# Optimization experiments

Measured on AMD Instinct MI355X. Metric: run time of the kernel, lower is better.

The kernel has to match this reference:

```python
import jax, jax.numpy as jnp
import numpy as np

T = 2048        # q_len (current chunk)
P = 2048        # past KV cache length
HID = 4096      # hidden_size
H = 32          # num_attention_heads
D = HID // H    # head_dim = 128
THETA = 10000.0


def apply_rope(x, pos):
    # x: [H, T, D], pos: [T] int
    half = D // 2
    inv_freq = 1.0 / (THETA ** (jnp.arange(0, half, dtype=jnp.float32) / half))
    ang = pos.astype(jnp.float32)[:, None] * inv_freq[None, :]      # [T, D/2]
    cos = jnp.concatenate([jnp.cos(ang), jnp.cos(ang)], axis=-1)[None]  # [1, T, D]
    sin = jnp.concatenate([jnp.sin(ang), jnp.sin(ang)], axis=-1)[None]
    rot = jnp.concatenate([-x[..., half:], x[..., :half]], axis=-1)
    return x * cos + rot * sin


def setup_inputs() -> dict:
    key = jax.random.key(0)
    ks = jax.random.split(key, 8)
    s = 1.0 / np.sqrt(HID)
    inp = {
        "hidden_states": jax.random.normal(ks[0], (T, HID), dtype=jnp.float32),
        "attention_mask": jnp.triu(jnp.full((T, T), -jnp.inf, dtype=jnp.float32), k=1),
        "Wq": jax.random.normal(ks[1], (HID, HID), dtype=jnp.float32) * s,
        "Wk": jax.random.normal(ks[2], (HID, HID), dtype=jnp.float32) * s,
        "Wv": jax.random.normal(ks[3], (HID, HID), dtype=jnp.float32) * s,
        "Wo": jax.random.normal(ks[4], (HID, HID), dtype=jnp.float32) * s,
        "past_k": jax.random.normal(ks[5], (H, P, D), dtype=jnp.float32),
        "past_v": jax.random.normal(ks[6], (H, P, D), dtype=jnp.float32),
        "position_ids": P + jnp.arange(T, dtype=jnp.int32),
        "past_length": P,
    }
    return inp


def reference(hidden_states, attention_mask, Wq, Wk, Wv, Wo, past_k, past_v,
              position_ids, past_length):
    # QKV projections -> [H, T, D]
    proj = lambda W: (hidden_states @ W).reshape(T, H, D).transpose(1, 0, 2)
    q, k, v = proj(Wq), proj(Wk), proj(Wv)
    q = apply_rope(q, position_ids)
    k = apply_rope(k, position_ids)

    scale = 1.0 / jnp.sqrt(jnp.float32(D))
    # scores against past cache and current chunk (fp32 softmax, as in source)
    past_dots = (jnp.einsum('htd,hsd->hts', q, past_k) * scale).astype(jnp.float32)
    pmask = jnp.where(jnp.arange(P) < past_length, 0.0, -jnp.inf)  # [P]
    past_dots = past_dots + pmask
    cur = ((jnp.einsum('htd,hsd->hts', q, k) * scale) + attention_mask).astype(jnp.float32)

    # online-softmax merge via logsumexp combination
    past_lse = jax.scipy.special.logsumexp(past_dots, axis=-1, keepdims=True)
    cur_lse = jax.scipy.special.logsumexp(cur, axis=-1, keepdims=True)
    tot_lse = jnp.logaddexp(past_lse, cur_lse)
    pw = jnp.exp(past_dots - tot_lse).astype(q.dtype)
    cw = jnp.exp(cur - tot_lse).astype(q.dtype)

    out = jnp.einsum('hts,hsd->htd', pw, past_v) + jnp.einsum('hts,hsd->htd', cw, v)
    out = jnp.where(past_length == 0,
                    jnp.einsum('hts,hsd->htd', jax.nn.softmax(cur, axis=-1).astype(q.dtype), v),
                    out)
    out = out.transpose(1, 0, 2).reshape(T, HID)   # [T, hidden]
    return out @ Wo
```

## Files before the change

### kernel.cpp

```cpp
#include <hip/hip_runtime.h>
#include <cstdint>
#include <cstddef>

#define T_LEN 2048
#define PAST_MAX 2048
#define HID 4096
#define NHEAD 32
#define DHEAD 128

typedef __bf16 bf16_t;
typedef __bf16 bf16x4 __attribute__((ext_vector_type(4)));
typedef __bf16 bf16x8 __attribute__((ext_vector_type(8)));
typedef float  f32x4  __attribute__((ext_vector_type(4)));
typedef float  f32x16 __attribute__((ext_vector_type(16)));
typedef unsigned int u32x4 __attribute__((ext_vector_type(4)));

__device__ __forceinline__ void gload16(const void* g, void* l){
  __builtin_amdgcn_global_load_lds((const __attribute__((address_space(1))) void*)g,
                                   (__attribute__((address_space(3))) void*)l,
                                   16, 0, 0);
}

__device__ __forceinline__ unsigned pack_bf16(float a, float b){
  const unsigned ua = __builtin_bit_cast(unsigned short, (bf16_t)a);
  const unsigned ub = __builtin_bit_cast(unsigned short, (bf16_t)b);
  return ua | (ub << 16);
}

__global__ void cvt2_k(const float* __restrict__ a, bf16_t* __restrict__ ao,
                       const float* __restrict__ b, bf16_t* __restrict__ bo, int n4){
  int i = blockIdx.x * 256 + threadIdx.x;
  if (i < n4){
    const float4 v = ((const float4*)a)[i];
    bf16x4 o = { (bf16_t)v.x, (bf16_t)v.y, (bf16_t)v.z, (bf16_t)v.w };
    ((bf16x4*)ao)[i] = o;
  } else {
    i -= n4;
    const float4 v = ((const float4*)b)[i];
    bf16x4 o = { (bf16_t)v.x, (bf16_t)v.y, (bf16_t)v.z, (bf16_t)v.w };
    ((bf16x4*)bo)[i] = o;
  }
}

__global__ __launch_bounds__(256) void transpose2_k(const float* __restrict__ in,
                                                    bf16_t* __restrict__ out, int R, int C){
  __shared__ float tile[64][65];
  const int r0 = blockIdx.x << 6, c0 = blockIdx.y << 6;
  const size_t bo = (size_t)blockIdx.z * (size_t)R * (size_t)C;
  const int tx = threadIdx.x & 15, ty = threadIdx.x >> 4;
#pragma unroll
  for (int k = 0; k < 4; ++k){
    const float4 v = *(const float4*)(in + bo + (size_t)(r0 + ty + 16*k) * C + c0 + tx*4);
    float* tp = &tile[ty + 16*k][tx*4];
    tp[0] = v.x; tp[1] = v.y; tp[2] = v.z; tp[3] = v.w;
  }
  __syncthreads();
  const int rr0 = (threadIdx.x & 7) * 8;
  const int ccb = threadIdx.x >> 3;
#pragma unroll
  for (int k = 0; k < 2; ++k){
    const int cc = ccb + 32*k;
    bf16x8 o;
#pragma unroll
    for (int j = 0; j < 8; ++j) o[j] = (bf16_t)tile[rr0 + j][cc];
    *(bf16x8*)(out + bo + (size_t)(c0 + cc) * R + r0 + rr0) = o;
  }
}

__global__ __launch_bounds__(256) void transpose3_k(
    const float* __restrict__ s0, const float* __restrict__ s1, const float* __restrict__ s2,
    bf16_t* __restrict__ d0, bf16_t* __restrict__ d1, bf16_t* __restrict__ d2){
  __shared__ float tile[64][65];
  const float* in = (blockIdx.z == 0) ? s0 : (blockIdx.z == 1) ? s1 : s2;
  bf16_t* out = (blockIdx.z == 0) ? d0 : (blockIdx.z == 1) ? d1 : d2;
  const int r0 = blockIdx.x << 6, c0 = blockIdx.y << 6;
  const int tx = threadIdx.x & 15, ty = threadIdx.x >> 4;
#pragma unroll
  for (int k = 0; k < 4; ++k){
    const float4 v = *(const float4*)(in + (size_t)(r0 + ty + 16*k) * HID + c0 + tx*4);
    float* tp = &tile[ty + 16*k][tx*4];
    tp[0] = v.x; tp[1] = v.y; tp[2] = v.z; tp[3] = v.w;
  }
  __syncthreads();
  const int rr0 = (threadIdx.x & 7) * 8;
  const int ccb = threadIdx.x >> 3;
#pragma unroll
  for (int k = 0; k < 2; ++k){
    const int cc = ccb + 32*k;
    bf16x8 o;
#pragma unroll
    for (int j = 0; j < 8; ++j) o[j] = (bf16_t)tile[rr0 + j][cc];
    *(bf16x8*)(out + (size_t)(c0 + cc) * HID + r0 + rr0) = o;
  }
}

__global__ void ropek8_k(bf16_t* __restrict__ K, const int* __restrict__ pos){
  const int idx = blockIdx.x * 256 + threadIdx.x;
  const int jc = idx & 7;
  const int t  = (idx >> 3) & (T_LEN - 1);
  const int h  = idx >> 14;
  const size_t base = ((size_t)h * T_LEN + t) * DHEAD;
  const float p = (float)pos[t];
  bf16x8 lo = *(bf16x8*)(K + base + jc * 8);
  bf16x8 hi = *(bf16x8*)(K + base + 64 + jc * 8);
  bf16x8 olo, ohi;
#pragma unroll
  for (int j = 0; j < 8; ++j){
    const int fi = jc * 8 + j;
    const float invf = __expf(-(float)fi * 0.14391156605212898f);
    float sn, cs;
    sincosf(p * invf, &sn, &cs);
    const float b0 = (float)lo[j], b1 = (float)hi[j];
    olo[j] = (bf16_t)(b0 * cs - b1 * sn);
    ohi[j] = (bf16_t)(b1 * cs + b0 * sn);
  }
  *(bf16x8*)(K + base + jc * 8) = olo;
  *(bf16x8*)(K + base + 64 + jc * 8) = ohi;
}

#define QUAD384(PR, BF) \
  __builtin_amdgcn_s_setprio(1); \
  _Pragma("unroll") \
  for (int kk = 0; kk < 2; ++kk){ \
    _Pragma("unroll") \
    for (int mf = 0; mf < 4; ++mf){ \
      _Pragma("unroll") \
      for (int ni = 0; ni < 2; ++ni) \
        acc[mf][(PR)*2 + ni] = __builtin_amdgcn_mfma_f32_16x16x32_bf16( \
            af[mf][kk], BF[ni][kk], acc[mf][(PR)*2 + ni], 0, 0, 0); \
    } \
  } \
  __builtin_amdgcn_s_setprio(0);

__global__ __launch_bounds__(512, 1) void gemmqkv384_k(
    const bf16_t* __restrict__ A,
    const bf16_t* __restrict__ Bc,
    bf16_t* __restrict__ OQ, bf16_t* __restrict__ OK2, bf16_t* __restrict__ OVT)
{
  const int bid = blockIdx.x;
  const int wg  = (bid & 7) * 64 + (bid >> 3);
  const int mt  = wg & 15;
  const int nt  = wg >> 4;
  const int m0  = mt << 7;
  const int n0g = nt * 384;

  const int tid = threadIdx.x;
  const int wv = tid >> 6, lane = tid & 63, lm = lane & 15, g = lane >> 4;
  const int wr = wv >> 2, wc = wv & 3;

  __shared__ __align__(16) char smem[131072];

  const f32x4 fzero = {0.f, 0.f, 0.f, 0.f};
  f32x4 acc[4][6];
#pragma unroll
  for (int i = 0; i < 4; ++i)
#pragma unroll
    for (int j = 0; j < 6; ++j) acc[i][j] = fzero;

  size_t aoff[2], boff[2];
#pragma unroll
  for (int i = 0; i < 2; ++i){
    const int c = i * 512 + tid;
    const int u = c >> 3;
    const int j = ((c & 7) ^ (u & 7)) << 3;
    aoff[i] = (size_t)(m0 + u) * HID + j;
    const int bcol = (u >> 5) * 96 + (u & 31);
    boff[i] = (size_t)(n0g + bcol) * HID + j;
  }
  const int ldst0 = (wv * 64) << 4;
  const int ldst1 = (512 + wv * 64) << 4;

  auto stgA = [&](char* buf, int kt){
    const bf16_t* src = A + (size_t)kt * 64;
    gload16(src + aoff[0], buf + ldst0);
    gload16(src + aoff[1], buf + ldst1);
  };
  auto stgB = [&](char* buf, int kt, int pr){
    const bf16_t* src = Bc + (size_t)kt * 64 + (size_t)pr * (32 * HID);
    char* dst = buf + 16384 + pr * 16384;
    gload16(src + boff[0], dst + ldst0);
    gload16(src + boff[1], dst + ldst1);
  };

  const int koff0 = ((0 + g) ^ (lm & 7)) << 4;
  const int koff1 = ((4 + g) ^ (lm & 7)) << 4;
  const int abase = ((wr << 6) + lm) << 7;
  const int bbase = ((wc << 5) + lm) << 7;

  stgA(smem, 0); stgB(smem, 0, 0); stgB(smem, 0, 1); stgB(smem, 0, 2);
  stgA(smem + 65536, 1); stgB(smem + 65536, 1, 0); stgB(smem + 65536, 1, 1);
  asm volatile("s_waitcnt vmcnt(6)" ::: "memory");
  __builtin_amdgcn_s_barrier();

  bf16x8 af[4][2], bf[2][2];

  for (int kt = 0; kt < 64; ++kt){
    char* buf  = smem + (kt & 1) * 65536;
    char* obuf = smem + ((kt + 1) & 1) * 65536;

#pragma unroll
    for (int mf = 0; mf < 4; ++mf){
      af[mf][0] = *(const bf16x8*)(buf + abase + mf * 2048 + koff0);
      af[mf][1] = *(const bf16x8*)(buf + abase + mf * 2048 + koff1);
    }
#pragma unroll
    for (int ni = 0; ni < 2; ++ni){
      bf[ni][0] = *(const bf16x8*)(buf + 16384 + bbase + ni * 2048 + koff0);
      bf[ni][1] = *(const bf16x8*)(buf + 16384 + bbase + ni * 2048 + koff1);
    }
    if (kt + 1 < 64) stgB(obuf, kt + 1, 2);
    __builtin_amdgcn_sched_barrier(0);
    __builtin_amdgcn_s_barrier();
    asm volatile("s_waitcnt lgkmcnt(0)" ::: "memory");
    __builtin_amdgcn_sched_barrier(0);
    QUAD384(0, bf)
    __builtin_amdgcn_s_barrier();

#pragma unroll
    for (int ni = 0; ni < 2; ++ni){
      bf[ni][0] = *(const bf16x8*)(buf + 32768 + bbase + ni * 2048 + koff0);
      bf[ni][1] = *(const bf16x8*)(buf + 32768 + bbase + ni * 2048 + koff1);
    }
    if (kt + 2 < 64) stgA(buf, kt + 2);
    __builtin_amdgcn_sched_barrier(0);
    __builtin_amdgcn_s_barrier();
    asm volatile("s_waitcnt lgkmcnt(0)" ::: "memory");
    __builtin_amdgcn_sched_barrier(0);
    QUAD384(1, bf)
    __builtin_amdgcn_s_barrier();

#pragma unroll
    for (int ni = 0; ni < 2; ++ni){
      bf[ni][0] = *(const bf16x8*)(buf + 49152 + bbase + ni * 2048 + koff0);
      bf[ni][1] = *(const bf16x8*)(buf + 49152 + bbase + ni * 2048 + koff1);
    }
    if (kt + 2 < 64){ stgB(buf, kt + 2, 0); stgB(buf, kt + 2, 1); }
    __builtin_amdgcn_sched_barrier(0);
    __builtin_amdgcn_s_barrier();
    asm volatile("s_waitcnt lgkmcnt(0)" ::: "memory");
    __builtin_amdgcn_sched_barrier(0);
    QUAD384(2, bf)
    if (kt <= 61) asm volatile("s_waitcnt vmcnt(6)" ::: "memory");
    else          asm volatile("s_waitcnt vmcnt(0)" ::: "memory");
    __builtin_amdgcn_sched_barrier(0);
    __builtin_amdgcn_s_barrier();
  }

#pragma unroll
  for (int pr = 0; pr < 3; ++pr)
#pragma unroll
    for (int ni = 0; ni < 2; ++ni){
      const int colg = n0g + wc * 96 + pr * 32 + ni * 16 + lm;
      const int z  = colg >> 12;
      const int wi = colg & 4095;
      const int hh = wi >> 7, dd = wi & 127;
      const int ai = pr * 2 + ni;
#pragma unroll
      for (int mf = 0; mf < 4; ++mf){
        const int trow0 = m0 + wr * 64 + mf * 16 + g * 4;
        if (z == 2){
          bf16x4 v4 = { (bf16_t)acc[mf][ai][0], (bf16_t)acc[mf][ai][1],
                        (bf16_t)acc[mf][ai][2], (bf16_t)acc[mf][ai][3] };
          *(bf16x4*)(OVT + ((size_t)hh * DHEAD + dd) * T_LEN + trow0) = v4;
        } else {
          bf16_t* ob = z ? OK2 : OQ;
#pragma unroll
          for (int r = 0; r < 4; ++r)
            ob[((size_t)hh * T_LEN + trow0 + r) * DHEAD + dd] = (bf16_t)acc[mf][ai][r];
        }
      }
    }
}

#define OPQUAD(PR, BF) \
  __builtin_amdgcn_s_setprio(1); \
  _Pragma("unroll") \
  for (int kk = 0; kk < 2; ++kk){ \
    _Pragma("unroll") \
    for (int mf = 0; mf < 4; ++mf){ \
      _Pragma("unroll") \
      for (int ni = 0; ni < 2; ++ni) \
        acc[mf][(PR)*2 + ni] = __builtin_amdgcn_mfma_f32_16x16x32_bf16( \
            af[mf][kk], BF[ni][kk], acc[mf][(PR)*2 + ni], 0, 0, 0); \
    } \
  } \
  __builtin_amdgcn_s_setprio(0);

__global__ __launch_bounds__(512, 1) void gemmop2p_k(
    const bf16_t* __restrict__ A, const bf16_t* __restrict__ B,
    float* __restrict__ OF)
{
  const int bid = blockIdx.x;
  const int wg  = (bid & 7) * 32 + (bid >> 3);
  const int mt  = wg & 15;
  const int nt  = wg >> 4;
  const int m0  = mt << 7;
  const int n0  = nt << 8;

  const int tid = threadIdx.x;
  const int wv = tid >> 6, lane = tid & 63, lm = lane & 15, g = lane >> 4;
  const int wr = wv >> 2, wc = wv & 3;

  __shared__ __align__(16) char smem[98304];

  const f32x4 fzero = {0.f, 0.f, 0.f, 0.f};
  f32x4 acc[4][4];
#pragma unroll
  for (int i = 0; i < 4; ++i)
#pragma unroll
    for (int j = 0; j < 4; ++j) acc[i][j] = fzero;

  size_t aoff[2], boff[2];
#pragma unroll
  for (int i = 0; i < 2; ++i){
    const int c = i * 512 + tid;
    const int u = c >> 3;
    const int j = ((c & 7) ^ (u & 7)) << 3;
    aoff[i] = (size_t)(m0 + u) * HID + j;
    const int bcol = (u >> 5) * 64 + (u & 31);
    boff[i] = (size_t)(n0 + bcol) * HID + j;
  }
  const int ldst0 = (wv * 64) << 4;
  const int ldst1 = (512 + wv * 64) << 4;

  auto stgA = [&](char* buf, int kt){
    const bf16_t* src = A + (size_t)kt * 64;
    gload16(src + aoff[0], buf + ldst0);
    gload16(src + aoff[1], buf + ldst1);
  };
  auto stgB = [&](char* buf, int kt, int pr){
    const bf16_t* src = B + (size_t)kt * 64 + (size_t)pr * (32 * HID);
    char* dst = buf + 16384 + pr * 16384;
    gload16(src + boff[0], dst + ldst0);
    gload16(src + boff[1], dst + ldst1);
  };

  const int koff0 = ((0 + g) ^ (lm & 7)) << 4;
  const int koff1 = ((4 + g) ^ (lm & 7)) << 4;
  const int abase = ((wr << 6) + lm) << 7;
  const int bbase = ((wc << 5) + lm) << 7;

  stgA(smem, 0); stgB(smem, 0, 0); stgB(smem, 0, 1);
  stgA(smem + 49152, 1); stgB(smem + 49152, 1, 0);
  asm volatile("s_waitcnt vmcnt(4)" ::: "memory");
  __builtin_amdgcn_s_barrier();

  bf16x8 af[4][2], bf[2][2];

  for (int kt = 0; kt < 64; ++kt){
    char* buf  = smem + (kt & 1) * 49152;
    char* obuf = smem + ((kt + 1) & 1) * 49152;

#pragma unroll
    for (int mf = 0; mf < 4; ++mf){
      af[mf][0] = *(const bf16x8*)(buf + abase + mf * 2048 + koff0);
      af[mf][1] = *(const bf16x8*)(buf + abase + mf * 2048 + koff1);
    }
#pragma unroll
    for (int ni = 0; ni < 2; ++ni){
      bf[ni][0] = *(const bf16x8*)(buf + 16384 + bbase + ni * 2048 + koff0);
      bf[ni][1] = *(const bf16x8*)(buf + 16384 + bbase + ni * 2048 + koff1);
    }
    if (kt + 1 < 64) stgB(obuf, kt + 1, 1);
    __builtin_amdgcn_sched_barrier(0);
    __builtin_amdgcn_s_barrier();
    asm volatile("s_waitcnt lgkmcnt(0)" ::: "memory");
    __builtin_amdgcn_sched_barrier(0);
    OPQUAD(0, bf)
    if (kt < 62) asm volatile("s_waitcnt vmcnt(6)" ::: "memory");
    else         asm volatile("s_waitcnt vmcnt(0)" ::: "memory");
    __builtin_amdgcn_sched_barrier(0);
    __builtin_amdgcn_s_barrier();

#pragma unroll
    for (int ni = 0; ni < 2; ++ni){
      bf[ni][0] = *(const bf16x8*)(buf + 32768 + bbase + ni * 2048 + koff0);
      bf[ni][1] = *(const bf16x8*)(buf + 32768 + bbase + ni * 2048 + koff1);
    }
    if (kt + 2 < 64){ stgA(buf, kt + 2); stgB(buf, kt + 2, 0); }
    __builtin_amdgcn_sched_barrier(0);
    __builtin_amdgcn_s_barrier();
    asm volatile("s_waitcnt lgkmcnt(0)" ::: "memory");
    __builtin_amdgcn_sched_barrier(0);
    OPQUAD(1, bf)
    if (kt < 62) asm volatile("s_waitcnt vmcnt(6)" ::: "memory");
    else         asm volatile("s_waitcnt vmcnt(0)" ::: "memory");
    __builtin_amdgcn_sched_barrier(0);
    __builtin_amdgcn_s_barrier();
  }

#pragma unroll
  for (int pr = 0; pr < 2; ++pr)
#pragma unroll
    for (int ni = 0; ni < 2; ++ni){
      const int col = n0 + wc * 64 + pr * 32 + ni * 16 + lm;
      const int ai = pr * 2 + ni;
#pragma unroll
      for (int mf = 0; mf < 4; ++mf)
#pragma unroll
        for (int r = 0; r < 4; ++r){
          const int trow = m0 + wr * 64 + mf * 16 + g * 4 + r;
          OF[(size_t)trow * HID + col] = acc[mf][ai][r];
        }
    }
}

__global__ __launch_bounds__(256, 2) void attn2_k(
    const bf16_t* __restrict__ Q,
    const bf16_t* __restrict__ Kc,
    const bf16_t* __restrict__ VTc,
    const bf16_t* __restrict__ Kp,
    const bf16_t* __restrict__ VTp,
    bf16_t* __restrict__ Ctx,
    const int* __restrict__ plen_p,
    const int* __restrict__ pos)
{
  const int bid = blockIdx.x;
  const int xcd = bid & 7;
  const int k   = bid >> 3;
  const int ho  = k >> 4;
  const int qraw= k & 15;
  const int h   = (xcd << 2) | ho;
  const int qb  = (ho & 2) ? (15 - qraw) : qraw;

  const int tid = threadIdx.x;
  const int w = tid >> 6, lane = tid & 63, l31 = lane & 31, hi = lane >> 5;
  const int qw0 = qb * 128 + w * 32;
  const int qrow = qw0 + l31;
  const int plen = plen_p[0];
  const int npast = (plen + 63) >> 6;
  const int NT = npast + 2 * qb + 2;

  __shared__ __align__(16) char smem[65536 + 512];
  float* lred = (float*)(smem + 65536);

  const bf16_t* qbase = Q + ((size_t)h * T_LEN + qrow) * DHEAD;
  bf16x8 qf[8];
#pragma unroll
  for (int dc = 0; dc < 8; ++dc)
    qf[dc] = *(const bf16x8*)(qbase + dc * 16 + 8 * hi);
  {
    const float ppos = (float)pos[qrow];
    const float qs = 0.08838834764831845f;
#pragma unroll
    for (int dc = 0; dc < 4; ++dc)
#pragma unroll
      for (int j = 0; j < 8; ++j){
        const int fi = dc * 16 + 8 * hi + j;
        const float invf = __expf(-(float)fi * 0.14391156605212898f);
        float sn, cs;
        sincosf(ppos * invf, &sn, &cs);
        const float a0 = (float)qf[dc][j], a1 = (float)qf[dc + 4][j];
        qf[dc][j]     = (bf16_t)((a0 * cs - a1 * sn) * qs);
        qf[dc + 4][j] = (bf16_t)((a1 * cs + a0 * sn) * qs);
      }
  }
  __builtin_amdgcn_sched_barrier(0);

  const f32x16 fz = {0.f,0.f,0.f,0.f,0.f,0.f,0.f,0.f,0.f,0.f,0.f,0.f,0.f,0.f,0.f,0.f};
  f32x16 o[4] = {fz, fz, fz, fz};
  float m = -1e30f, l = 0.f;

  auto stage = [&](int t, int buf){
    const bf16_t* kb; const bf16_t* vb;
    if (t < npast){
      const int s0 = t * 64;
      kb = Kp  + ((size_t)h * PAST_MAX + s0) * DHEAD;
      vb = VTp + (size_t)h * DHEAD * PAST_MAX + s0;
    } else {
      const int s0 = (t - npast) * 64;
      kb = Kc  + ((size_t)h * T_LEN + s0) * DHEAD;
      vb = VTc + (size_t)h * DHEAD * T_LEN + s0;
    }
    char* kl = smem + buf * 32768;
    char* vl = kl + 16384;
#pragma unroll
    for (int i = 0; i < 4; ++i){
      const int c = i * 256 + w * 64 + lane;
      const int krow = c >> 4, kcol = c & 15;
      gload16(kb + (size_t)krow * DHEAD + ((kcol ^ (krow & 7)) << 3), kl + (i * 256 + w * 64) * 16);
      const int vrow = c >> 3, vcol = c & 7;
      gload16(vb + (size_t)vrow * 2048 + ((vcol ^ (vrow & 7)) << 3), vl + (i * 256 + w * 64) * 16);
    }
  };

  stage(0, 0);
  __builtin_amdgcn_sched_barrier(0);

  for (int t = 0; t < NT; ++t){
    const int cur = t & 1;
    if (t + 1 < NT){
      stage(t + 1, cur ^ 1);
      asm volatile("s_waitcnt vmcnt(8)" ::: "memory");
    } else {
      asm volatile("s_waitcnt vmcnt(0)" ::: "memory");
    }
    __builtin_amdgcn_sched_barrier(0);
    __builtin_amdgcn_s_barrier();
    __builtin_amdgcn_sched_barrier(0);

    const bool isc = (t >= npast);
    const int s0c = (t - npast) * 64;
    const bool active = !isc || (s0c <= qw0 + 31);

    if (active){
      char* kl = smem + cur * 32768;
      char* vl = kl + 16384;

      f32x16 sacc[2] = {fz, fz};
      __builtin_amdgcn_s_setprio(1);
#pragma unroll
      for (int kvh = 0; kvh < 2; ++kvh){
        const int krow = (kvh << 5) + l31;
        const int kbo = krow << 8;
        const int sw = (krow & 7) << 4;
#pragma unroll
        for (int dc = 0; dc < 8; ++dc){
          const bf16x8 kf = *(const bf16x8*)(kl + kbo + ((dc * 32 + 16 * hi) ^ sw));
          sacc[kvh] = __builtin_amdgcn_mfma_f32_32x32x16_bf16(kf, qf[dc], sacc[kvh], 0, 0, 0);
        }
      }
      __builtin_amdgcn_s_setprio(0);

      const bool mcur  = isc && (s0c + 63 > qw0);
      const bool mpast = !isc && ((t + 1) * 64 > plen);
      float pv[2][16];
      float pm = -1e30f;
      if (mcur | mpast){
#pragma unroll
        for (int kvh = 0; kvh < 2; ++kvh)
#pragma unroll
          for (int r = 0; r < 16; ++r){
            float x = sacc[kvh][r];
            const int kvoff = (kvh << 5) + (r & 3) + 8 * (r >> 2) + 4 * hi;
            if (mcur  && (s0c + kvoff >  qrow)) x = -1e30f;
            if (mpast && (t * 64 + kvoff >= plen)) x = -1e30f;
            pv[kvh][r] = x;
            pm = fmaxf(pm, x);
          }
      } else {
#pragma unroll
        for (int kvh = 0; kvh < 2; ++kvh)
#pragma unroll
          for (int r = 0; r < 16; ++r){
            pv[kvh][r] = sacc[kvh][r];
            pm = fmaxf(pm, sacc[kvh][r]);
          }
      }
      pm = fmaxf(pm, __shfl_xor(pm, 32));

      if (!__all(pm - m <= 8.f)){
        const float mn = fmaxf(m, pm);
        const float corr = __expf(m - mn);
        m = mn;
        l *= corr;
        if (hi == 0) lred[(w << 5) + l31] = corr;
        asm volatile("s_waitcnt lgkmcnt(0)" ::: "memory");
#pragma unroll
        for (int r = 0; r < 16; ++r){
          const float cc = lred[(w << 5) + (r & 3) + 8 * (r >> 2) + 4 * hi];
#pragma unroll
          for (int nb = 0; nb < 4; ++nb) o[nb][r] *= cc;
        }
      }

      float sum = 0.f;
#pragma unroll
      for (int kvh = 0; kvh < 2; ++kvh)
#pragma unroll
        for (int r = 0; r < 16; ++r){
          const float pe = __expf(pv[kvh][r] - m);
          pv[kvh][r] = pe;
          sum += pe;
        }
      sum += __shfl_xor(sum, 32);
      l += sum;

      unsigned wds[2][8];
#pragma unroll
      for (int kvh = 0; kvh < 2; ++kvh)
#pragma unroll
        for (int i = 0; i < 8; ++i)
          wds[kvh][i] = pack_bf16(pv[kvh][2 * i], pv[kvh][2 * i + 1]);

      bf16x8 pf[4];
#pragma unroll
      for (int ks = 0; ks < 4; ++ks){
        const int s = ks & 1, kvh = ks >> 1;
        const unsigned a0 = hi ? wds[kvh][4 * s]     : wds[kvh][4 * s + 2];
        const unsigned a1 = hi ? wds[kvh][4 * s + 1] : wds[kvh][4 * s + 3];
        const unsigned z0 = (unsigned)__shfl_xor((int)a0, 32);
        const unsigned z1 = (unsigned)__shfl_xor((int)a1, 32);
        u32x4 fw;
        fw[0] = hi ? z0 : wds[kvh][4 * s];
        fw[1] = hi ? z1 : wds[kvh][4 * s + 1];
        fw[2] = hi ? wds[kvh][4 * s + 2] : z0;
        fw[3] = hi ? wds[kvh][4 * s + 3] : z1;
        pf[ks] = __builtin_bit_cast(bf16x8, fw);
      }

      __builtin_amdgcn_s_setprio(1);
#pragma unroll
      for (int ks = 0; ks < 4; ++ks)
#pragma unroll
        for (int nb = 0; nb < 4; ++nb){
          const int vrow = (nb << 5) + l31;
          const bf16x8 vf = *(const bf16x8*)(vl + (vrow << 7) + ((ks * 32 + 16 * hi) ^ ((vrow & 7) << 4)));
          o[nb] = __builtin_amdgcn_mfma_f32_32x32x16_bf16(pf[ks], vf, o[nb], 0, 0, 0);
        }
      __builtin_amdgcn_s_setprio(0);
    }
    __builtin_amdgcn_sched_barrier(0);
    __builtin_amdgcn_s_barrier();
  }

  if (hi == 0) lred[(w << 5) + l31] = l;
  asm volatile("s_waitcnt lgkmcnt(0)" ::: "memory");
#pragma unroll
  for (int r = 0; r < 16; ++r){
    const int cr = (r & 3) + 8 * (r >> 2) + 4 * hi;
    const float li = 1.f / lred[(w << 5) + cr];
    const int trow = qw0 + cr;
    bf16_t* cb = Ctx + (size_t)trow * HID + h * DHEAD + l31;
#pragma unroll
    for (int nb = 0; nb < 4; ++nb)
      cb[nb << 5] = (bf16_t)(o[nb][r] * li);
  }
}

extern "C" void kernel_launch(void* const* d_in, const int* in_sizes, int n_in,
                              void* d_out, int out_size, void* d_ws, size_t ws_size,
                              hipStream_t stream)
{
  const float* X   = (const float*)d_in[0];
  const float* Wq  = (const float*)d_in[2];
  const float* Wk  = (const float*)d_in[3];
  const float* Wv  = (const float*)d_in[4];
  const float* Wo  = (const float*)d_in[5];
  const float* PKi = (const float*)d_in[6];
  const float* PVi = (const float*)d_in[7];
  const int* POS   = (const int*)d_in[8];
  const int* PLEN  = (const int*)d_in[9];
  float* OUT = (float*)d_out;

  char* ws = (char*)d_ws;
  const size_t SZ_XB  = (size_t)T_LEN * HID * 2;
  const size_t SZ_W   = (size_t)HID * HID * 2;
  const size_t SZ_HTD = (size_t)NHEAD * T_LEN * DHEAD * 2;

  bf16_t* XB  = (bf16_t*)(ws);
  bf16_t* WT0 = (bf16_t*)(ws + SZ_XB);
  bf16_t* WT1 = (bf16_t*)(ws + SZ_XB + SZ_W);
  bf16_t* WT2 = (bf16_t*)(ws + SZ_XB + 2 * SZ_W);
  char* p = ws + SZ_XB + 3 * SZ_W;
  bf16_t* QB   = (bf16_t*)p; p += SZ_HTD;
  bf16_t* KB   = (bf16_t*)p; p += SZ_HTD;
  bf16_t* VTB  = (bf16_t*)p; p += SZ_HTD;
  bf16_t* KPB  = (bf16_t*)p; p += SZ_HTD;
  bf16_t* VPTB = (bf16_t*)p; p += SZ_HTD;
  bf16_t* CTX  = (bf16_t*)p; p += SZ_HTD;
  bf16_t* WOT  = QB;

  dim3 blk256(256);
  dim3 blk512(512);
  cvt2_k<<<16384, blk256, 0, stream>>>(X, XB, PKi, KPB, T_LEN * HID / 4);
  transpose3_k<<<dim3(64,64,3), blk256, 0, stream>>>(Wq, Wk, Wv, WT0, WT1, WT2);
  transpose2_k<<<dim3(32,2,32), blk256, 0, stream>>>(PVi, VPTB, PAST_MAX, DHEAD);

  gemmqkv384_k<<<512, blk512, 0, stream>>>(XB, WT0, QB, KB, VTB);
  ropek8_k<<<2048, blk256, 0, stream>>>(KB, POS);
  attn2_k<<<512, blk256, 0, stream>>>(QB, KB, VTB, KPB, VPTB, CTX, PLEN, POS);

  transpose2_k<<<dim3(64,64,1), blk256, 0, stream>>>(Wo, WOT, HID, HID);
  gemmop2p_k<<<256, blk512, 0, stream>>>(CTX, WOT, OUT);
}
```

Before: 539.2 us.

## Software-pipeline QKV GEMM with double-buffered register fragments across LDS phases

Restructures the fused QKV GEMM main loop into a two-k-tile unrolled, six-phase pipeline. It uses ping-pong register sets for the A and B fragments, so LDS reads for the next phase are issued before the current MFMA block runs, with partial lgkmcnt waits instead of full drains. Global-to-LDS staging is redistributed across phases and bounds-guarded, and the final iteration is peeled. The aim is to hide LDS read latency behind MFMA work, at the cost of more registers and a more fragile wait-count schedule.

```diff
diff --git a/kernel.cpp b/kernel.cpp
--- a/kernel.cpp
+++ b/kernel.cpp
@@ -118,7 +118,7 @@
   *(bf16x8*)(K + base + 64 + jc * 8) = ohi;
 }
 
-#define QUAD384(PR, BF) \
+#define MM6(AF, BF, PR) \
   __builtin_amdgcn_s_setprio(1); \
   _Pragma("unroll") \
   for (int kk = 0; kk < 2; ++kk){ \
@@ -127,12 +127,42 @@
       _Pragma("unroll") \
       for (int ni = 0; ni < 2; ++ni) \
         acc[mf][(PR)*2 + ni] = __builtin_amdgcn_mfma_f32_16x16x32_bf16( \
-            af[mf][kk], BF[ni][kk], acc[mf][(PR)*2 + ni], 0, 0, 0); \
+            AF[mf][kk], BF[ni][kk], acc[mf][(PR)*2 + ni], 0, 0, 0); \
     } \
   } \
-  __builtin_amdgcn_s_setprio(0);
-
-__global__ __launch_bounds__(512, 1) void gemmqkv384_k(
+  __builtin_amdgcn_s_setprio(0); \
+  __builtin_amdgcn_sched_barrier(0);
+
+#define RDA(SET, BUF) \
+  _Pragma("unroll") \
+  for (int mf = 0; mf < 4; ++mf){ \
+    SET[mf][0] = *(const bf16x8*)((BUF) + abase + mf * 2048 + koff0); \
+    SET[mf][1] = *(const bf16x8*)((BUF) + abase + mf * 2048 + koff1); \
+  }
+
+#define RDB(SET, BUF, UOFF) \
+  _Pragma("unroll") \
+  for (int ni = 0; ni < 2; ++ni){ \
+    SET[ni][0] = *(const bf16x8*)((BUF) + (UOFF) + bbase + ni * 2048 + koff0); \
+    SET[ni][1] = *(const bf16x8*)((BUF) + (UOFF) + bbase + ni * 2048 + koff1); \
+  }
+
+#define PTOP8 \
+  asm volatile("s_waitcnt vmcnt(8)" ::: "memory"); \
+  __builtin_amdgcn_s_barrier(); \
+  __builtin_amdgcn_sched_barrier(0);
+
+#define PTOP0 \
+  asm volatile("s_waitcnt vmcnt(0)" ::: "memory"); \
+  __builtin_amdgcn_s_barrier(); \
+  __builtin_amdgcn_sched_barrier(0);
+
+#define LGK(N) \
+  __builtin_amdgcn_sched_barrier(0); \
+  asm volatile("s_waitcnt lgkmcnt(" #N ")" ::: "memory"); \
+  __builtin_amdgcn_sched_barrier(0);
+
+__global__ __launch_bounds__(512, 1) void gemmqkv6p_k(
     const bf16_t* __restrict__ A,
     const bf16_t* __restrict__ Bc,
     bf16_t* __restrict__ OQ, bf16_t* __restrict__ OK2, bf16_t* __restrict__ OVT)
@@ -149,6 +179,8 @@
   const int wr = wv >> 2, wc = wv & 3;
 
   __shared__ __align__(16) char smem[131072];
+  char* const buf0 = smem;
+  char* const buf1 = smem + 65536;
 
   const f32x4 fzero = {0.f, 0.f, 0.f, 0.f};
   f32x4 acc[4][6];
@@ -171,15 +203,19 @@
   const int ldst1 = (512 + wv * 64) << 4;
 
   auto stgA = [&](char* buf, int kt){
-    const bf16_t* src = A + (size_t)kt * 64;
-    gload16(src + aoff[0], buf + ldst0);
-    gload16(src + aoff[1], buf + ldst1);
+    if ((unsigned)kt < 64u){
+      const bf16_t* src = A + (size_t)kt * 64;
+      gload16(src + aoff[0], buf + ldst0);
+      gload16(src + aoff[1], buf + ldst1);
+    }
   };
   auto stgB = [&](char* buf, int kt, int pr){
-    const bf16_t* src = Bc + (size_t)kt * 64 + (size_t)pr * (32 * HID);
-    char* dst = buf + 16384 + pr * 16384;
-    gload16(src + boff[0], dst + ldst0);
-    gload16(src + boff[1], dst + ldst1);
+    if ((unsigned)kt < 64u){
+      const bf16_t* src = Bc + (size_t)kt * 64 + (size_t)pr * (32 * HID);
+      char* dst = buf + 16384 + pr * 16384;
+      gload16(src + boff[0], dst + ldst0);
+      gload16(src + boff[1], dst + ldst1);
+    }
   };
 
   const int koff0 = ((0 + g) ^ (lm & 7)) << 4;
@@ -187,64 +223,75 @@
   const int abase = ((wr << 6) + lm) << 7;
   const int bbase = ((wc << 5) + lm) << 7;
 
-  stgA(smem, 0); stgB(smem, 0, 0); stgB(smem, 0, 1); stgB(smem, 0, 2);
-  stgA(smem + 65536, 1); stgB(smem + 65536, 1, 0); stgB(smem + 65536, 1, 1);
+  stgA(buf0, 0); stgB(buf0, 0, 0); stgB(buf0, 0, 1); stgB(buf0, 0, 2);
+  stgA(buf1, 1); stgB(buf1, 1, 0); stgB(buf1, 1, 1);
   asm volatile("s_waitcnt vmcnt(6)" ::: "memory");
   __builtin_amdgcn_s_barrier();
 
-  bf16x8 af[4][2], bf[2][2];
-
-  for (int kt = 0; kt < 64; ++kt){
-    char* buf  = smem + (kt & 1) * 65536;
-    char* obuf = smem + ((kt + 1) & 1) * 65536;
-
-#pragma unroll
-    for (int mf = 0; mf < 4; ++mf){
-      af[mf][0] = *(const bf16x8*)(buf + abase + mf * 2048 + koff0);
-      af[mf][1] = *(const bf16x8*)(buf + abase + mf * 2048 + koff1);
-    }
-#pragma unroll
-    for (int ni = 0; ni < 2; ++ni){
-      bf[ni][0] = *(const bf16x8*)(buf + 16384 + bbase + ni * 2048 + koff0);
-      bf[ni][1] = *(const bf16x8*)(buf + 16384 + bbase + ni * 2048 + koff1);
-    }
-    if (kt + 1 < 64) stgB(obuf, kt + 1, 2);
-    __builtin_amdgcn_sched_barrier(0);
-    __builtin_amdgcn_s_barrier();
-    asm volatile("s_waitcnt lgkmcnt(0)" ::: "memory");
-    __builtin_amdgcn_sched_barrier(0);
-    QUAD384(0, bf)
-    __builtin_amdgcn_s_barrier();
-
-#pragma unroll
-    for (int ni = 0; ni < 2; ++ni){
-      bf[ni][0] = *(const bf16x8*)(buf + 32768 + bbase + ni * 2048 + koff0);
-      bf[ni][1] = *(const bf16x8*)(buf + 32768 + bbase + ni * 2048 + koff1);
-    }
-    if (kt + 2 < 64) stgA(buf, kt + 2);
-    __builtin_amdgcn_sched_barrier(0);
-    __builtin_amdgcn_s_barrier();
-    asm volatile("s_waitcnt lgkmcnt(0)" ::: "memory");
-    __builtin_amdgcn_sched_barrier(0);
-    QUAD384(1, bf)
-    __builtin_amdgcn_s_barrier();
-
-#pragma unroll
-    for (int ni = 0; ni < 2; ++ni){
-      bf[ni][0] = *(const bf16x8*)(buf + 49152 + bbase + ni * 2048 + koff0);
-      bf[ni][1] = *(const bf16x8*)(buf + 49152 + bbase + ni * 2048 + koff1);
-    }
-    if (kt + 2 < 64){ stgB(buf, kt + 2, 0); stgB(buf, kt + 2, 1); }
-    __builtin_amdgcn_sched_barrier(0);
-    __builtin_amdgcn_s_barrier();
-    asm volatile("s_waitcnt lgkmcnt(0)" ::: "memory");
-    __builtin_amdgcn_sched_barrier(0);
-    QUAD384(2, bf)
-    if (kt <= 61) asm volatile("s_waitcnt vmcnt(6)" ::: "memory");
-    else          asm volatile("s_waitcnt vmcnt(0)" ::: "memory");
-    __builtin_amdgcn_sched_barrier(0);
-    __builtin_amdgcn_s_barrier();
-  }
+  bf16x8 afA[4][2], afB[4][2], bU[2][2], bV[2][2];
+  RDA(afA, buf0)
+  RDB(bU, buf0, 16384)
+
+  for (int i = 0; i < 31; ++i){
+    const int kt0 = 2 * i;
+    PTOP8
+    RDB(bV, buf0, 32768)
+    stgB(buf1, kt0 + 1, 2);
+    LGK(4)
+    MM6(afA, bU, 0)
+    PTOP8
+    RDB(bU, buf0, 49152)
+    stgA(buf0, kt0 + 2); stgB(buf0, kt0 + 2, 0);
+    LGK(4)
+    MM6(afA, bV, 1)
+    PTOP8
+    RDA(afB, buf1)
+    RDB(bV, buf1, 16384)
+    stgB(buf0, kt0 + 2, 1);
+    LGK(12)
+    MM6(afA, bU, 2)
+    PTOP8
+    RDB(bU, buf1, 32768)
+    stgB(buf0, kt0 + 2, 2);
+    LGK(4)
+    MM6(afB, bV, 0)
+    PTOP8
+    RDB(bV, buf1, 49152)
+    stgA(buf1, kt0 + 3); stgB(buf1, kt0 + 3, 0);
+    LGK(4)
+    MM6(afB, bU, 1)
+    PTOP8
+    RDA(afA, buf0)
+    RDB(bU, buf0, 16384)
+    stgB(buf1, kt0 + 3, 1);
+    LGK(12)
+    MM6(afB, bV, 2)
+  }
+
+  PTOP0
+  RDB(bV, buf0, 32768)
+  stgB(buf1, 63, 2);
+  LGK(4)
+  MM6(afA, bU, 0)
+  PTOP0
+  RDB(bU, buf0, 49152)
+  LGK(4)
+  MM6(afA, bV, 1)
+  PTOP0
+  RDA(afB, buf1)
+  RDB(bV, buf1, 16384)
+  LGK(12)
+  MM6(afA, bU, 2)
+  PTOP0
+  RDB(bU, buf1, 32768)
+  LGK(4)
+  MM6(afB, bV, 0)
+  PTOP0
+  RDB(bV, buf1, 49152)
+  LGK(4)
+  MM6(afB, bU, 1)
+  LGK(0)
+  MM6(afB, bV, 2)
 
 #pragma unroll
   for (int pr = 0; pr < 3; ++pr)
@@ -667,7 +714,7 @@
   transpose3_k<<<dim3(64,64,3), blk256, 0, stream>>>(Wq, Wk, Wv, WT0, WT1, WT2);
   transpose2_k<<<dim3(32,2,32), blk256, 0, stream>>>(PVi, VPTB, PAST_MAX, DHEAD);
 
-  gemmqkv384_k<<<512, blk512, 0, stream>>>(XB, WT0, QB, KB, VTB);
+  gemmqkv6p_k<<<512, blk512, 0, stream>>>(XB, WT0, QB, KB, VTB);
   ropek8_k<<<2048, blk256, 0, stream>>>(KB, POS);
   attn2_k<<<512, blk256, 0, stream>>>(QB, KB, VTB, KPB, VPTB, CTX, PLEN, POS);
 
```

After: 530.1 us. No clear change (-1.7%).
